# Kernel tuning notes

Measured on AMD Instinct MI355X. Metric: run time of the kernel, lower is better.

## Reference

```python
import jax, jax.numpy as jnp
import numpy as np

VOCAB = 50000
D = 512          # sru output_dim (input_size == hidden_size)
L = 2            # n_sru_layers
B = 8
T = 2048


def setup_inputs() -> dict:
    key = jax.random.key(0)
    ks = jax.random.split(key, 6)
    ids = jax.random.randint(ks[0], (B, T), 0, VOCAB)
    # ragged valid lengths -> mask True = real token, False = pad
    lens = jax.random.randint(ks[1], (B,), T // 2, T + 1)
    mask = jnp.arange(T)[None, :] < lens[:, None]
    emb = jax.random.normal(ks[2], (VOCAB, D), jnp.float32) * 0.02
    # per-layer SRU params: W projects to (x_tilde, f, r); v = peephole weight_c; b = gate biases
    Ws = jax.random.normal(ks[3], (L, D, 3 * D), jnp.float32) / np.sqrt(D)
    vs = jax.random.normal(ks[4], (L, 2 * D), jnp.float32) * 0.1
    bs = jnp.zeros((L, 2 * D), jnp.float32)
    return {"ids": ids, "mask": mask, "emb": emb, "Ws": Ws, "vs": vs, "bs": bs}


def _sru_layer(x, W, v, b, pad):
    # x: [T,B,D] time-major, pad: [T,B] True where padded
    Tn, Bn, d = x.shape
    U = jnp.einsum('tbd,de->tbe', x, W).reshape(Tn, Bn, 3, d)
    vf, vr = v[:d], v[d:]
    bf, br = b[:d], b[d:]

    def step(c, inp):
        xt, u, m = inp                      # xt:[B,d] u:[B,3,d] m:[B]
        u0, u1, u2 = u[:, 0], u[:, 1], u[:, 2]
        f = jax.nn.sigmoid(u1 + vf * c + bf)
        r = jax.nn.sigmoid(u2 + vr * c + br)
        c_new = f * c + (1.0 - f) * u0
        h = r * jnp.tanh(c_new) + (1.0 - r) * xt   # highway (input==hidden)
        m_ = m[:, None]
        c_out = jnp.where(m_, c, c_new)     # padded steps keep state
        h = jnp.where(m_, 0.0, h)           # and emit zeros
        return c_out, h

    c0 = jnp.zeros((Bn, d), x.dtype)
    _, hs = jax.lax.scan(step, c0, (x, U, pad))
    return hs


def reference(ids, mask, emb, Ws, vs, bs):
    x = emb[ids]                     # char embedder -> [B,T,D]
    x = jnp.transpose(x, (1, 0, 2))  # [T,B,D]
    pad = (~mask).T                  # inverted mask, transposed -> [T,B]
    for l in range(Ws.shape[0]):
        x = _sru_layer(x, Ws[l], vs[l], bs[l], pad)
    return jnp.transpose(x, (1, 0, 2))  # back to [B,T,D]
```

## Files before the change

### kernel.cpp

```cpp
#include <hip/hip_runtime.h>
#include <hip/hip_bf16.h>

#define D 512
#define L_LAYERS 2
#define BATCH 8
#define TT 2048
#define N3 1536
#define REC 4096
#define HALF_IDX (1024 * 1024)

typedef __attribute__((ext_vector_type(8))) short short8;
typedef __attribute__((ext_vector_type(4))) float floatx4;

#if __has_builtin(__builtin_amdgcn_exp2f)
#define EXP2F(x) __builtin_amdgcn_exp2f(x)
#else
#define EXP2F(x) exp2f(x)
#endif
#if __has_builtin(__builtin_amdgcn_rcpf)
#define RCPF(x) __builtin_amdgcn_rcpf(x)
#else
#define RCPF(x) (1.0f / (x))
#endif

__device__ __forceinline__ unsigned short f2bf(float f) {
  unsigned u = __builtin_bit_cast(unsigned, f);
  u += 0x7FFFu + ((u >> 16) & 1u);
  return (unsigned short)(u >> 16);
}

__global__ __launch_bounds__(128) void embed_kernel(const int* __restrict__ ids,
                                                    const float* __restrict__ emb,
                                                    unsigned short* __restrict__ xa) {
  int bt = blockIdx.x;
  int b = bt >> 11;
  int t = bt & 2047;
  int id = ids[bt];
  int d = threadIdx.x << 2;
  const float4 v = *(const float4*)(emb + (size_t)id * D + d);
  ushort4 w;
  w.x = f2bf(v.x); w.y = f2bf(v.y); w.z = f2bf(v.z); w.w = f2bf(v.w);
  *(ushort4*)(xa + ((size_t)t * BATCH + b) * D + d) = w;
}

__global__ __launch_bounds__(256) void wconv_kernel(const float* __restrict__ Ws,
                                                    unsigned short* __restrict__ Wt,
                                                    const void* __restrict__ maskp,
                                                    int* __restrict__ lenb) {
  if (blockIdx.x == 0 && threadIdx.x >= 248) {
    int b = threadIdx.x - 248;
    int w0 = *(const int*)maskp;
    int mode = (w0 == 1) ? 0 : ((w0 == 0x01010101) ? 1 : 2);
    int lo = 0, hi = TT;
    while (lo < hi) {
      int mid = (lo + hi) >> 1;
      int idx = b * TT + mid;
      bool mm = (mode == 0) ? (((const int*)maskp)[idx] != 0)
              : (mode == 1) ? (((const unsigned char*)maskp)[idx] != 0)
                            : (((const float*)maskp)[idx] != 0.f);
      if (mm) lo = mid + 1; else hi = mid;
    }
    lenb[b] = lo;
  }
  int idx = blockIdx.x * 256 + threadIdx.x;
  if (idx >= L_LAYERS * D * N3) return;
  int n = idx % N3;
  int k = (idx / N3) % D;
  int l = idx / (N3 * D);
  Wt[((size_t)l * N3 + n) * D + k] = f2bf(Ws[idx]);
}

__device__ __forceinline__ void gemm_body(int bi, int bm_base,
                                          const unsigned short* __restrict__ A,
                                          const unsigned short* __restrict__ Bt,
                                          unsigned* __restrict__ Ua32,
                                          unsigned short* __restrict__ Uc16,
                                          unsigned short* As,
                                          unsigned short* Bs) {
  constexpr int K = D;
  int tid = threadIdx.x;
  int lane = tid & 63;
  int wave = tid >> 6;
  int xcd = bi & 7;
  int j = bi >> 3;
  int bm = bm_base + xcd * 8 + (j >> 2);
  int dc0 = (j & 3) * 128;
  int m0 = bm * 128;
  int wm = (wave & 1) * 64;
  int w2 = wave >> 1;
  int q = lane >> 4, r16 = lane & 15;

  int arow = tid >> 2;
  int aoff = (tid & 3) * 8;
  int nsrc[3];
#pragma unroll
  for (int i = 0; i < 3; ++i) {
    int c = arow + i * 128;
    int g = c >> 4;
    int p = g % 3;
    int dcol = (g / 3) * 16 + (c & 15);
    nsrc[i] = dc0 + dcol + p * 512;
  }
  const unsigned short* asrc = A + (size_t)(m0 + arow) * K + aoff;

  floatx4 acc[4][6] = {};

#define GSTAGE(bufi, k0s)                                                                  \
  {                                                                                        \
    __builtin_amdgcn_global_load_lds(                                                      \
        (const __attribute__((address_space(1))) unsigned int*)(asrc + (k0s)),             \
        (__attribute__((address_space(3))) unsigned int*)(As + (bufi) * 4096 + tid * 8), 16, 0, 0); \
    _Pragma("unroll")                                                                      \
    for (int i = 0; i < 3; ++i) {                                                          \
      __builtin_amdgcn_global_load_lds(                                                    \
          (const __attribute__((address_space(1))) unsigned int*)(Bt + (size_t)nsrc[i] * K + (k0s) + aoff), \
          (__attribute__((address_space(3))) unsigned int*)(Bs + (bufi) * 12288 + i * 4096 + tid * 8), 16, 0, 0); \
    }                                                                                      \
  }

  GSTAGE(0, 0);
  __syncthreads();
  int cur = 0;
  for (int k0 = 0; k0 < K; k0 += 32) {
    if (k0 + 32 < K) GSTAGE(cur ^ 1, k0 + 32);
    short8 af[4], bfr[6];
#pragma unroll
    for (int i = 0; i < 4; ++i)
      af[i] = *(const short8*)&As[cur * 4096 + (wm + i * 16 + r16) * 32 + q * 8];
#pragma unroll
    for (int i = 0; i < 6; ++i)
      bfr[i] = *(const short8*)&Bs[cur * 12288 + (w2 * 96 + i * 16 + r16) * 32 + q * 8];
#pragma unroll
    for (int mi = 0; mi < 4; ++mi)
#pragma unroll
      for (int ni = 0; ni < 6; ++ni)
        acc[mi][ni] = __builtin_amdgcn_mfma_f32_16x16x32_bf16(af[mi], bfr[ni], acc[mi][ni], 0, 0, 0);
    __syncthreads();
    cur ^= 1;
  }
#undef GSTAGE

#pragma unroll
  for (int mi = 0; mi < 4; ++mi)
#pragma unroll
    for (int half = 0; half < 2; ++half) {
      int dcol = dc0 + w2 * 32 + half * 16 + r16;
#pragma unroll
      for (int i = 0; i < 4; ++i) {
        int m = m0 + wm + mi * 16 + q * 4 + i;
        size_t rec = (size_t)m * D + dcol;
        unsigned ua = (unsigned)f2bf(acc[mi][half * 3 + 0][i]) |
                      ((unsigned)f2bf(acc[mi][half * 3 + 1][i]) << 16);
        Ua32[rec] = ua;
        Uc16[rec] = f2bf(acc[mi][half * 3 + 2][i]);
      }
    }
}

__device__ __forceinline__ void chain_body(unsigned* __restrict__ Uac,
                                           const float* __restrict__ vsl,
                                           const float* __restrict__ bsl,
                                           const int* __restrict__ lenb,
                                           float* __restrict__ csave,
                                           int ch, int t0, int t1) {
  int b = ch >> 9;
  int d = ch & 511;
  int len = lenb[b];
  const float NL2E = -1.4426950408889634f;
  float vfe = NL2E * vsl[d];
  float cbf = NL2E * bsl[d];
  const unsigned* pa = Uac + ch;
  float* pc = (float*)Uac + ch;
  int nact = (len + 31) >> 5;
  int kbeg = t0 >> 5;
  int kend = t1 >> 5;
  if (nact < kend) kend = nact;

  unsigned uA[32], uB[32];

#define CLOAD(k, u)                                         \
  _Pragma("unroll") for (int j = 0; j < 32; ++j)            \
      u[j] = pa[(size_t)((k) * 32 + j) * REC];

#define CCOMP(k, u)                                         \
  _Pragma("unroll") for (int j = 0; j < 32; ++j) {          \
    unsigned a = u[j];                                      \
    float u0 = __builtin_bit_cast(float, a << 16);          \
    float u1f = __builtin_bit_cast(float, a & 0xFFFF0000u); \
    float k1 = fmaf(u1f, NL2E, cbf);                        \
    float a2 = fmaf(vfe, c, k1);                            \
    float e = EXP2F(a2);                                    \
    float inv = RCPF(e + 1.f);                              \
    c = fmaf(c - u0, inv, u0);                              \
    pc[(size_t)((k) * 32 + j) * REC] = c;                   \
  }

  float c = (t0 == 0) ? 0.f : csave[ch];
  if (kbeg < kend) {
    CLOAD(kbeg, uA);
    int k = kbeg;
    for (;;) {
      if (k + 1 < kend) CLOAD(k + 1, uB);
      CCOMP(k, uA);
      if (++k >= kend) break;
      if (k + 1 < kend) CLOAD(k + 1, uA);
      CCOMP(k, uB);
      if (++k >= kend) break;
    }
  }
#undef CLOAD
#undef CCOMP
  if (t1 < TT) csave[ch] = c;
}

template <bool LAST>
__device__ __forceinline__ void hpost_body(int idx,
                                           const unsigned short* __restrict__ Uc,
                                           const unsigned short* __restrict__ Xin,
                                           const float4* __restrict__ cq,
                                           const float* __restrict__ vsl,
                                           const float* __restrict__ bsl,
                                           const int* __restrict__ lenb,
                                           unsigned short* __restrict__ Hout,
                                           float* __restrict__ Out) {
  int t = idx >> 10;
  int q = idx & 1023;
  int rec0 = q << 2;
  int b = rec0 >> 9;
  int d = rec0 & 511;
  int len = lenb[b];
  ushort4 uv = *(const ushort4*)(Uc + (size_t)idx * 4);
  ushort4 xv = *(const ushort4*)(Xin + (size_t)idx * 4);
  float4 ct = cq[idx];
  float4 cp = (t > 0) ? cq[idx - 1024] : make_float4(0.f, 0.f, 0.f, 0.f);
  float4 vr4 = *(const float4*)(vsl + D + d);
  float4 br4 = *(const float4*)(bsl + D + d);
  const float NL2E = -1.4426950408889634f;
  const float L2E2 = 2.8853900817779268f;
  unsigned uu[4] = {uv.x, uv.y, uv.z, uv.w};
  unsigned xx[4] = {xv.x, xv.y, xv.z, xv.w};
  float cta[4] = {ct.x, ct.y, ct.z, ct.w};
  float cpa[4] = {cp.x, cp.y, cp.z, cp.w};
  float vra[4] = {vr4.x, vr4.y, vr4.z, vr4.w};
  float bra[4] = {br4.x, br4.y, br4.z, br4.w};
  bool act = t < len;
  float h[4];
#pragma unroll
  for (int j = 0; j < 4; ++j) {
    float u2 = __builtin_bit_cast(float, uu[j] << 16);
    float xf = __builtin_bit_cast(float, xx[j] << 16);
    float k2 = fmaf(u2, NL2E, NL2E * bra[j]);
    float a2 = fmaf(NL2E * vra[j], cpa[j], k2);
    float r = RCPF(EXP2F(a2) + 1.f);
    float et = EXP2F(cta[j] * L2E2);
    float th = fmaf(-2.f, RCPF(et + 1.f), 1.f);
    float hv = fmaf(r, th - xf, xf);
    h[j] = act ? hv : 0.f;
  }
  if (LAST) {
    *(float4*)(Out + ((size_t)b * TT + t) * D + d) = make_float4(h[0], h[1], h[2], h[3]);
  } else {
    ushort4 o; o.x = f2bf(h[0]); o.y = f2bf(h[1]); o.z = f2bf(h[2]); o.w = f2bf(h[3]);
    *(ushort4*)(Hout + (size_t)idx * 4) = o;
  }
}

__global__ __launch_bounds__(512) void gemm_kernel(const unsigned short* __restrict__ A,
                                                   const unsigned short* __restrict__ Bt,
                                                   unsigned* __restrict__ Ua32,
                                                   unsigned short* __restrict__ Uc16,
                                                   int bm_base) {
  __shared__ __align__(16) unsigned short As[2 * 4096];
  __shared__ __align__(16) unsigned short Bs[2 * 12288];
  gemm_body(blockIdx.x, bm_base, A, Bt, Ua32, Uc16, As, Bs);
}

__global__ __launch_bounds__(512) void gc_kernel(const unsigned short* __restrict__ A,
                                                 const unsigned short* __restrict__ Bt,
                                                 unsigned* __restrict__ Ua32,
                                                 unsigned short* __restrict__ Uc16,
                                                 const float* __restrict__ vsl,
                                                 const float* __restrict__ bsl,
                                                 const int* __restrict__ lenb,
                                                 float* __restrict__ csave) {
  __shared__ __align__(16) unsigned short As[2 * 4096];
  __shared__ __align__(16) unsigned short Bs[2 * 12288];
  int bi = blockIdx.x;
  if (bi < 64) {
    if (threadIdx.x >= 64) return;
    chain_body(Ua32, vsl, bsl, lenb, csave, bi * 64 + threadIdx.x, 0, 1024);
  } else {
    gemm_body(bi - 64, 64, A, Bt, Ua32, Uc16, As, Bs);
  }
}

template <bool LAST>
__global__ __launch_bounds__(256) void ch_kernel(unsigned* __restrict__ Uac,
                                                 const unsigned short* __restrict__ Uc,
                                                 const unsigned short* __restrict__ Xin,
                                                 const float* __restrict__ vsl,
                                                 const float* __restrict__ bsl,
                                                 const int* __restrict__ lenb,
                                                 float* __restrict__ csave,
                                                 unsigned short* __restrict__ Hout,
                                                 float* __restrict__ Out) {
  int bi = blockIdx.x;
  if (bi < 64) {
    if (threadIdx.x >= 64) return;
    chain_body(Uac, vsl, bsl, lenb, csave, bi * 64 + threadIdx.x, 1024, 2048);
  } else {
    hpost_body<LAST>((bi - 64) * 256 + threadIdx.x, Uc, Xin, (const float4*)Uac,
                     vsl, bsl, lenb, Hout, Out);
  }
}

template <bool LAST>
__global__ __launch_bounds__(256) void hpost_kernel(const unsigned short* __restrict__ Uc,
                                                    const unsigned short* __restrict__ Xin,
                                                    const float4* __restrict__ cq,
                                                    const float* __restrict__ vsl,
                                                    const float* __restrict__ bsl,
                                                    const int* __restrict__ lenb,
                                                    unsigned short* __restrict__ Hout,
                                                    float* __restrict__ Out) {
  hpost_body<LAST>(HALF_IDX + blockIdx.x * 256 + threadIdx.x, Uc, Xin, cq,
                   vsl, bsl, lenb, Hout, Out);
}

extern "C" void kernel_launch(void* const* d_in, const int* in_sizes, int n_in,
                              void* d_out, int out_size, void* d_ws, size_t ws_size,
                              hipStream_t stream) {
  const int* ids = (const int*)d_in[0];
  const void* mask = d_in[1];
  const float* emb = (const float*)d_in[2];
  const float* Ws = (const float*)d_in[3];
  const float* vs = (const float*)d_in[4];
  const float* bs = (const float*)d_in[5];
  float* out = (float*)d_out;

  char* ws = (char*)d_ws;
  unsigned short* Ua = (unsigned short*)ws;
  unsigned short* Uc = Ua + (size_t)TT * REC * 2;
  unsigned short* xa = Uc + (size_t)TT * REC;
  unsigned short* xb = xa + (size_t)TT * REC;
  unsigned short* Wt = xb + (size_t)TT * REC;
  int* lenb = (int*)(Wt + (size_t)L_LAYERS * D * N3);
  float* csave = (float*)(lenb + 16);

  embed_kernel<<<BATCH * TT, 128, 0, stream>>>(ids, emb, xa);
  wconv_kernel<<<(L_LAYERS * D * N3 + 255) / 256, 256, 0, stream>>>(Ws, Wt, mask, lenb);

  gemm_kernel<<<256, 512, 0, stream>>>(xa, Wt, (unsigned*)Ua, Uc, 0);
  gc_kernel<<<320, 512, 0, stream>>>(xa, Wt, (unsigned*)Ua, Uc, vs, bs, lenb, csave);
  ch_kernel<false><<<4160, 256, 0, stream>>>((unsigned*)Ua, Uc, xa, vs, bs, lenb,
                                             csave, xb, nullptr);
  hpost_kernel<false><<<4096, 256, 0, stream>>>(Uc, xa, (const float4*)Ua,
                                                vs, bs, lenb, xb, nullptr);
  gemm_kernel<<<256, 512, 0, stream>>>(xb, Wt + (size_t)N3 * D, (unsigned*)Ua, Uc, 0);
  gc_kernel<<<320, 512, 0, stream>>>(xb, Wt + (size_t)N3 * D, (unsigned*)Ua, Uc,
                                     vs + 2 * D, bs + 2 * D, lenb, csave);
  ch_kernel<true><<<4160, 256, 0, stream>>>((unsigned*)Ua, Uc, xb, vs + 2 * D, bs + 2 * D,
                                            lenb, csave, nullptr, out);
  hpost_kernel<true><<<4096, 256, 0, stream>>>(Uc, xb, (const float4*)Ua,
                                               vs + 2 * D, bs + 2 * D, lenb, nullptr, out);
}
```

Before: 405.6 us.

## Overlap layer-1 GEMM with layer-0 tail hpost and shrink GEMM M-tile

Merges the embedding and weight-conversion kernels into one launch. Halves the GEMM block M-tile from 128 to 64 rows, so each wave now holds 4x3 accumulators and the grid doubles. Runs the second-half layer-0 hpost in the same kernel as the first-half layer-1 GEMM, since they touch disjoint rows, which removes a launch and lets the two overlap. The recurrent chain threads also raise their wave priority so the serial scan is favoured over co-resident GEMM waves. The cost is more B-tile reloads per output from the smaller M tile and a more complex launch schedule.

```diff
diff --git a/kernel.cpp b/kernel.cpp
--- a/kernel.cpp
+++ b/kernel.cpp
@@ -29,26 +29,29 @@
   return (unsigned short)(u >> 16);
 }
 
-__global__ __launch_bounds__(128) void embed_kernel(const int* __restrict__ ids,
-                                                    const float* __restrict__ emb,
-                                                    unsigned short* __restrict__ xa) {
-  int bt = blockIdx.x;
-  int b = bt >> 11;
-  int t = bt & 2047;
-  int id = ids[bt];
-  int d = threadIdx.x << 2;
-  const float4 v = *(const float4*)(emb + (size_t)id * D + d);
-  ushort4 w;
-  w.x = f2bf(v.x); w.y = f2bf(v.y); w.z = f2bf(v.z); w.w = f2bf(v.w);
-  *(ushort4*)(xa + ((size_t)t * BATCH + b) * D + d) = w;
-}
-
-__global__ __launch_bounds__(256) void wconv_kernel(const float* __restrict__ Ws,
-                                                    unsigned short* __restrict__ Wt,
-                                                    const void* __restrict__ maskp,
-                                                    int* __restrict__ lenb) {
-  if (blockIdx.x == 0 && threadIdx.x >= 248) {
-    int b = threadIdx.x - 248;
+__global__ __launch_bounds__(256) void ew_kernel(const int* __restrict__ ids,
+                                                 const float* __restrict__ emb,
+                                                 unsigned short* __restrict__ xa,
+                                                 const float* __restrict__ Ws,
+                                                 unsigned short* __restrict__ Wt,
+                                                 const void* __restrict__ maskp,
+                                                 int* __restrict__ lenb) {
+  int bi = blockIdx.x;
+  int tid = threadIdx.x;
+  if (bi < 8192) {
+    int bt = bi * 2 + (tid >> 7);
+    int b = bt >> 11;
+    int t = bt & 2047;
+    int id = ids[bt];
+    int d = (tid & 127) << 2;
+    const float4 v = *(const float4*)(emb + (size_t)id * D + d);
+    ushort4 w;
+    w.x = f2bf(v.x); w.y = f2bf(v.y); w.z = f2bf(v.z); w.w = f2bf(v.w);
+    *(ushort4*)(xa + ((size_t)t * BATCH + b) * D + d) = w;
+    return;
+  }
+  if (bi == 8192 && tid >= 248) {
+    int b = tid - 248;
     int w0 = *(const int*)maskp;
     int mode = (w0 == 1) ? 0 : ((w0 == 0x01010101) ? 1 : 2);
     int lo = 0, hi = TT;
@@ -62,7 +65,7 @@
     }
     lenb[b] = lo;
   }
-  int idx = blockIdx.x * 256 + threadIdx.x;
+  int idx = (bi - 8192) * 256 + tid;
   if (idx >= L_LAYERS * D * N3) return;
   int n = idx % N3;
   int k = (idx / N3) % D;
@@ -83,11 +86,9 @@
   int wave = tid >> 6;
   int xcd = bi & 7;
   int j = bi >> 3;
-  int bm = bm_base + xcd * 8 + (j >> 2);
+  int bm = bm_base + xcd * 16 + (j >> 2);
   int dc0 = (j & 3) * 128;
-  int m0 = bm * 128;
-  int wm = (wave & 1) * 64;
-  int w2 = wave >> 1;
+  int m0 = bm * 64;
   int q = lane >> 4, r16 = lane & 15;
 
   int arow = tid >> 2;
@@ -101,15 +102,16 @@
     int dcol = (g / 3) * 16 + (c & 15);
     nsrc[i] = dc0 + dcol + p * 512;
   }
-  const unsigned short* asrc = A + (size_t)(m0 + arow) * K + aoff;
-
-  floatx4 acc[4][6] = {};
+  const unsigned short* asrc = A + (size_t)(m0 + (tid >> 2)) * K + aoff;
+
+  floatx4 acc[4][3] = {};
 
 #define GSTAGE(bufi, k0s)                                                                  \
   {                                                                                        \
-    __builtin_amdgcn_global_load_lds(                                                      \
-        (const __attribute__((address_space(1))) unsigned int*)(asrc + (k0s)),             \
-        (__attribute__((address_space(3))) unsigned int*)(As + (bufi) * 4096 + tid * 8), 16, 0, 0); \
+    if (tid < 256)                                                                         \
+      __builtin_amdgcn_global_load_lds(                                                    \
+          (const __attribute__((address_space(1))) unsigned int*)(asrc + (k0s)),           \
+          (__attribute__((address_space(3))) unsigned int*)(As + (bufi) * 2048 + tid * 8), 16, 0, 0); \
     _Pragma("unroll")                                                                      \
     for (int i = 0; i < 3; ++i) {                                                          \
       __builtin_amdgcn_global_load_lds(                                                    \
@@ -123,37 +125,34 @@
   int cur = 0;
   for (int k0 = 0; k0 < K; k0 += 32) {
     if (k0 + 32 < K) GSTAGE(cur ^ 1, k0 + 32);
-    short8 af[4], bfr[6];
+    short8 af[4], bfr[3];
 #pragma unroll
     for (int i = 0; i < 4; ++i)
-      af[i] = *(const short8*)&As[cur * 4096 + (wm + i * 16 + r16) * 32 + q * 8];
-#pragma unroll
-    for (int i = 0; i < 6; ++i)
-      bfr[i] = *(const short8*)&Bs[cur * 12288 + (w2 * 96 + i * 16 + r16) * 32 + q * 8];
+      af[i] = *(const short8*)&As[cur * 2048 + (i * 16 + r16) * 32 + q * 8];
+#pragma unroll
+    for (int i = 0; i < 3; ++i)
+      bfr[i] = *(const short8*)&Bs[cur * 12288 + (wave * 48 + i * 16 + r16) * 32 + q * 8];
 #pragma unroll
     for (int mi = 0; mi < 4; ++mi)
 #pragma unroll
-      for (int ni = 0; ni < 6; ++ni)
+      for (int ni = 0; ni < 3; ++ni)
         acc[mi][ni] = __builtin_amdgcn_mfma_f32_16x16x32_bf16(af[mi], bfr[ni], acc[mi][ni], 0, 0, 0);
     __syncthreads();
     cur ^= 1;
   }
 #undef GSTAGE
 
+  int dcol = dc0 + wave * 16 + r16;
 #pragma unroll
   for (int mi = 0; mi < 4; ++mi)
 #pragma unroll
-    for (int half = 0; half < 2; ++half) {
-      int dcol = dc0 + w2 * 32 + half * 16 + r16;
-#pragma unroll
-      for (int i = 0; i < 4; ++i) {
-        int m = m0 + wm + mi * 16 + q * 4 + i;
-        size_t rec = (size_t)m * D + dcol;
-        unsigned ua = (unsigned)f2bf(acc[mi][half * 3 + 0][i]) |
-                      ((unsigned)f2bf(acc[mi][half * 3 + 1][i]) << 16);
-        Ua32[rec] = ua;
-        Uc16[rec] = f2bf(acc[mi][half * 3 + 2][i]);
-      }
+    for (int i = 0; i < 4; ++i) {
+      int m = m0 + mi * 16 + q * 4 + i;
+      size_t rec = (size_t)m * D + dcol;
+      unsigned ua = (unsigned)f2bf(acc[mi][0][i]) |
+                    ((unsigned)f2bf(acc[mi][1][i]) << 16);
+      Ua32[rec] = ua;
+      Uc16[rec] = f2bf(acc[mi][2][i]);
     }
 }
 
@@ -163,6 +162,7 @@
                                            const int* __restrict__ lenb,
                                            float* __restrict__ csave,
                                            int ch, int t0, int t1) {
+  __builtin_amdgcn_s_setprio(1);
   int b = ch >> 9;
   int d = ch & 511;
   int len = lenb[b];
@@ -211,6 +211,7 @@
 #undef CLOAD
 #undef CCOMP
   if (t1 < TT) csave[ch] = c;
+  __builtin_amdgcn_s_setprio(0);
 }
 
 template <bool LAST>
@@ -270,7 +271,7 @@
                                                    unsigned* __restrict__ Ua32,
                                                    unsigned short* __restrict__ Uc16,
                                                    int bm_base) {
-  __shared__ __align__(16) unsigned short As[2 * 4096];
+  __shared__ __align__(16) unsigned short As[2 * 2048];
   __shared__ __align__(16) unsigned short Bs[2 * 12288];
   gemm_body(blockIdx.x, bm_base, A, Bt, Ua32, Uc16, As, Bs);
 }
@@ -283,14 +284,14 @@
                                                  const float* __restrict__ bsl,
                                                  const int* __restrict__ lenb,
                                                  float* __restrict__ csave) {
-  __shared__ __align__(16) unsigned short As[2 * 4096];
+  __shared__ __align__(16) unsigned short As[2 * 2048];
   __shared__ __align__(16) unsigned short Bs[2 * 12288];
   int bi = blockIdx.x;
   if (bi < 64) {
     if (threadIdx.x >= 64) return;
     chain_body(Ua32, vsl, bsl, lenb, csave, bi * 64 + threadIdx.x, 0, 1024);
   } else {
-    gemm_body(bi - 64, 64, A, Bt, Ua32, Uc16, As, Bs);
+    gemm_body(bi - 64, 128, A, Bt, Ua32, Uc16, As, Bs);
   }
 }
 
@@ -314,17 +315,37 @@
   }
 }
 
-template <bool LAST>
-__global__ __launch_bounds__(256) void hpost_kernel(const unsigned short* __restrict__ Uc,
+__global__ __launch_bounds__(512) void hg_kernel(const unsigned short* __restrict__ Uc,
+                                                 const unsigned short* __restrict__ Xin,
+                                                 const unsigned* __restrict__ UacPrev,
+                                                 const float* __restrict__ vsl0,
+                                                 const float* __restrict__ bsl0,
+                                                 const int* __restrict__ lenb,
+                                                 unsigned short* __restrict__ Hout,
+                                                 const unsigned short* __restrict__ A1,
+                                                 const unsigned short* __restrict__ Bt1,
+                                                 unsigned* __restrict__ Ua32,
+                                                 unsigned short* __restrict__ Uc16) {
+  __shared__ __align__(16) unsigned short As[2 * 2048];
+  __shared__ __align__(16) unsigned short Bs[2 * 12288];
+  int bi = blockIdx.x;
+  if (bi < 2048) {
+    hpost_body<false>(HALF_IDX + bi * 512 + threadIdx.x, Uc, Xin,
+                      (const float4*)UacPrev, vsl0, bsl0, lenb, Hout, nullptr);
+  } else {
+    gemm_body(bi - 2048, 0, A1, Bt1, Ua32, Uc16, As, Bs);
+  }
+}
+
+__global__ __launch_bounds__(512) void hpost_kernel(const unsigned short* __restrict__ Uc,
                                                     const unsigned short* __restrict__ Xin,
                                                     const float4* __restrict__ cq,
                                                     const float* __restrict__ vsl,
                                                     const float* __restrict__ bsl,
                                                     const int* __restrict__ lenb,
-                                                    unsigned short* __restrict__ Hout,
                                                     float* __restrict__ Out) {
-  hpost_body<LAST>(HALF_IDX + blockIdx.x * 256 + threadIdx.x, Uc, Xin, cq,
-                   vsl, bsl, lenb, Hout, Out);
+  hpost_body<true>(HALF_IDX + blockIdx.x * 512 + threadIdx.x, Uc, Xin, cq,
+                   vsl, bsl, lenb, nullptr, Out);
 }
 
 extern "C" void kernel_launch(void* const* d_in, const int* in_sizes, int n_in,
@@ -347,20 +368,20 @@
   int* lenb = (int*)(Wt + (size_t)L_LAYERS * D * N3);
   float* csave = (float*)(lenb + 16);
 
-  embed_kernel<<<BATCH * TT, 128, 0, stream>>>(ids, emb, xa);
-  wconv_kernel<<<(L_LAYERS * D * N3 + 255) / 256, 256, 0, stream>>>(Ws, Wt, mask, lenb);
-
-  gemm_kernel<<<256, 512, 0, stream>>>(xa, Wt, (unsigned*)Ua, Uc, 0);
-  gc_kernel<<<320, 512, 0, stream>>>(xa, Wt, (unsigned*)Ua, Uc, vs, bs, lenb, csave);
+  const unsigned short* Wt1 = Wt + (size_t)N3 * D;
+
+  ew_kernel<<<14336, 256, 0, stream>>>(ids, emb, xa, Ws, Wt, mask, lenb);
+
+  gemm_kernel<<<512, 512, 0, stream>>>(xa, Wt, (unsigned*)Ua, Uc, 0);
+  gc_kernel<<<576, 512, 0, stream>>>(xa, Wt, (unsigned*)Ua, Uc, vs, bs, lenb, csave);
   ch_kernel<false><<<4160, 256, 0, stream>>>((unsigned*)Ua, Uc, xa, vs, bs, lenb,
                                              csave, xb, nullptr);
-  hpost_kernel<false><<<4096, 256, 0, stream>>>(Uc, xa, (const float4*)Ua,
-                                                vs, bs, lenb, xb, nullptr);
-  gemm_kernel<<<256, 512, 0, stream>>>(xb, Wt + (size_t)N3 * D, (unsigned*)Ua, Uc, 0);
-  gc_kernel<<<320, 512, 0, stream>>>(xb, Wt + (size_t)N3 * D, (unsigned*)Ua, Uc,
+  hg_kernel<<<2560, 512, 0, stream>>>(Uc, xa, (const unsigned*)Ua, vs, bs, lenb, xb,
+                                      xb, Wt1, (unsigned*)Ua, Uc);
+  gc_kernel<<<576, 512, 0, stream>>>(xb, Wt1, (unsigned*)Ua, Uc,
                                      vs + 2 * D, bs + 2 * D, lenb, csave);
   ch_kernel<true><<<4160, 256, 0, stream>>>((unsigned*)Ua, Uc, xb, vs + 2 * D, bs + 2 * D,
                                             lenb, csave, nullptr, out);
-  hpost_kernel<true><<<4096, 256, 0, stream>>>(Uc, xb, (const float4*)Ua,
-                                               vs + 2 * D, bs + 2 * D, lenb, nullptr, out);
-}
+  hpost_kernel<<<2048, 512, 0, stream>>>(Uc, xb, (const float4*)Ua,
+                                         vs + 2 * D, bs + 2 * D, lenb, out);
+}
```

New measurement: 417.1 us. +2.8%, slower.
